# Optimization experiments

Hardware: AMD Instinct MI355X
Metric: run time of the kernel (lower is better)

Reference implementation:

```python
import jax, jax.numpy as jnp
import numpy as np

ODE_UNFOLDS = 6
EPS = 1e-8
MOTOR = 64  # wiring.output_dim


def setup_inputs() -> dict:
    key = jax.random.key(0)
    ks = jax.random.split(key, 16)
    B, S, U = 128, 128, 512  # batch, sensory_size, units
    d = {}
    d["inputs"] = jax.random.normal(ks[0], (B, S), jnp.float32)
    d["state"] = 0.1 * jax.random.normal(ks[1], (B, U), jnp.float32)
    # init ranges from LTCCell._init_ranges
    d["gleak"] = jax.random.uniform(ks[2], (U,), jnp.float32, 0.001, 1.0)
    d["vleak"] = jax.random.uniform(ks[3], (U,), jnp.float32, -0.2, 0.2)
    d["cm"] = jax.random.uniform(ks[4], (U,), jnp.float32, 0.4, 0.6)
    d["sigma"] = jax.random.uniform(ks[5], (U, U), jnp.float32, 3.0, 8.0)
    d["mu"] = jax.random.uniform(ks[6], (U, U), jnp.float32, 0.3, 0.8)
    d["w"] = jax.random.uniform(ks[7], (U, U), jnp.float32, 0.001, 1.0)
    d["erev"] = jnp.where(jax.random.uniform(ks[8], (U, U)) < 0.5, -1.0, 1.0).astype(jnp.float32)
    d["sensory_sigma"] = jax.random.uniform(ks[9], (S, U), jnp.float32, 3.0, 8.0)
    d["sensory_mu"] = jax.random.uniform(ks[10], (S, U), jnp.float32, 0.3, 0.8)
    d["sensory_w"] = jax.random.uniform(ks[11], (S, U), jnp.float32, 0.001, 1.0)
    d["sensory_erev"] = jnp.where(jax.random.uniform(ks[12], (S, U)) < 0.5, -1.0, 1.0).astype(jnp.float32)
    # affine input/output mapping params (initialized to identity as in build())
    d["input_w"] = jnp.ones((S,), jnp.float32)
    d["input_b"] = jnp.zeros((S,), jnp.float32)
    d["output_w"] = jnp.ones((MOTOR,), jnp.float32)
    d["output_b"] = jnp.zeros((MOTOR,), jnp.float32)
    d["sparsity_mask"] = (jax.random.uniform(ks[13], (U, U)) < 0.5).astype(jnp.float32)
    d["sensory_sparsity_mask"] = (jax.random.uniform(ks[14], (S, U)) < 0.5).astype(jnp.float32)
    return d


def reference(inputs, state, gleak, vleak, cm, sigma, mu, w, erev,
              sensory_sigma, sensory_mu, sensory_w, sensory_erev,
              input_w, input_b, output_w, output_b,
              sparsity_mask, sensory_sparsity_mask):
    # _map_inputs (affine)
    x = inputs * input_w + input_b  # [B, S]
    # sensory synapse activation (computed once, outside the unfold loop)
    # [B, S, U] = w * sigmoid((v_pre - mu) * sigma) * mask
    sens_act = sensory_w * jax.nn.sigmoid((x[:, :, None] - sensory_mu) * sensory_sigma) * sensory_sparsity_mask
    w_num_sensory = jnp.sum(sens_act * sensory_erev, axis=1)  # [B, U]
    w_den_sensory = jnp.sum(sens_act, axis=1)                 # [B, U]
    # cm_t = cm / (elapsed_time / ode_unfolds), elapsed_time = 1.0
    cm_t = cm * jnp.float32(ODE_UNFOLDS)

    def step(v_pre, _):
        # [B, U, U]
        act = w * jax.nn.sigmoid((v_pre[:, :, None] - mu) * sigma) * sparsity_mask
        w_num = jnp.sum(act * erev, axis=1) + w_num_sensory
        w_den = jnp.sum(act, axis=1) + w_den_sensory
        numerator = cm_t * v_pre + gleak * vleak + w_num
        denominator = cm_t + gleak + w_den
        return numerator / (denominator + EPS), None

    next_state, _ = jax.lax.scan(step, state, None, length=ODE_UNFOLDS)
    # _map_outputs: slice motor neurons, then affine
    outputs = next_state[:, :MOTOR] * output_w + output_b
    return outputs, next_state
```

## Files before the change

### kernel.cpp

```cpp
#include <hip/hip_runtime.h>

#define BATCH 128
#define SENS 128
#define UNITS 512
#define MOTOR 64
#define UNFOLDS 6
#define L2E 1.442695040888963f
#define EPS 1e-8f

#define BT 8
#define UT 8
#define STP 12

__global__ __launch_bounds__(256) void fold_kernel(
    const float* __restrict__ sigma, const float* __restrict__ mu,
    const float* __restrict__ w, const float* __restrict__ erev,
    const float* __restrict__ mask,
    const float* __restrict__ ssig, const float* __restrict__ smu,
    const float* __restrict__ sw, const float* __restrict__ serev,
    const float* __restrict__ smask,
    const float* __restrict__ inputs, const float* __restrict__ input_w,
    const float* __restrict__ input_b,
    float4* __restrict__ pw4, float4* __restrict__ ps4,
    float* __restrict__ x)
{
    int i = blockIdx.x * 256 + threadIdx.x;
    if (i < UNITS * UNITS) {
        float sg = sigma[i] * L2E;
        float wmv = w[i] * mask[i];
        float4 q;
        q.x = sg; q.y = mu[i] * sg; q.z = wmv; q.w = wmv * erev[i];
        pw4[i] = q;
    }
    if (i < SENS * UNITS) {
        float sg = ssig[i] * L2E;
        float wmv = sw[i] * smask[i];
        float4 q;
        q.x = sg; q.y = smu[i] * sg; q.z = wmv; q.w = wmv * serev[i];
        ps4[i] = q;
    }
    if (i < BATCH * SENS) {
        int s = i & (SENS - 1);
        x[i] = __builtin_fmaf(inputs[i], input_w[s], input_b[s]);
    }
}

__global__ __launch_bounds__(256, 4) void sensory_kernel(
    const float* __restrict__ x,
    const float4* __restrict__ ps4,
    float* __restrict__ wns, float* __restrict__ wds)
{
    __shared__ __align__(16) float xsT[SENS][STP];
    __shared__ float2 red[4][BT][UT];

    int phys = blockIdx.x;
    int logical = (phys & 7) * 128 + (phys >> 3);
    int ut = logical >> 4;
    int bt = logical & 15;
    int b0 = bt * BT;
    int u0 = ut * UT;

    {
        const float4* xv = (const float4*)(x + b0 * SENS);
        int bl = threadIdx.x & 7;
        int s4 = threadIdx.x >> 3;
        float4 t = xv[bl * (SENS / 4) + s4];
        xsT[s4 * 4 + 0][bl] = t.x;
        xsT[s4 * 4 + 1][bl] = t.y;
        xsT[s4 * 4 + 2][bl] = t.z;
        xsT[s4 * 4 + 3][bl] = t.w;
    }
    __syncthreads();

    int ul = threadIdx.x & 7;
    int ss = threadIdx.x >> 3;
    int u = u0 + ul;

    float num[BT], den[BT];
    #pragma unroll
    for (int b = 0; b < BT; ++b) { num[b] = 0.f; den[b] = 0.f; }

    const float4* pv = ps4 + (size_t)ss * UNITS + u;
    const float* srow = &xsT[ss][0];
    #pragma unroll
    for (int i = 0; i < SENS / 32; ++i) {
        float4 q = pv[0];
        pv += 32 * UNITS;
        const float4* sp = (const float4*)srow;
        float4 xa = sp[0];
        float4 xb = sp[1];
        srow += 32 * STP;
        float sarr[8] = {xa.x, xa.y, xa.z, xa.w, xb.x, xb.y, xb.z, xb.w};
        #pragma unroll
        for (int b = 0; b < BT; ++b) {
            float t = __builtin_fmaf(-sarr[b], q.x, q.y);
            float e = __builtin_amdgcn_exp2f(t);
            float sg = __builtin_amdgcn_rcpf(1.0f + e);
            num[b] = __builtin_fmaf(q.w, sg, num[b]);
            den[b] = __builtin_fmaf(q.z, sg, den[b]);
        }
    }

    #pragma unroll
    for (int b = 0; b < BT; ++b) {
        #pragma unroll
        for (int m = 8; m <= 32; m <<= 1) {
            num[b] += __shfl_xor(num[b], m, 64);
            den[b] += __shfl_xor(den[b], m, 64);
        }
    }
    int lane = threadIdx.x & 63;
    int wid = threadIdx.x >> 6;
    if (lane < 8) {
        #pragma unroll
        for (int b = 0; b < BT; ++b)
            red[wid][b][lane] = make_float2(num[b], den[b]);
    }
    __syncthreads();
    if (threadIdx.x < 64) {
        int uu = threadIdx.x & 7;
        int bb = threadIdx.x >> 3;
        float n = 0.f, d = 0.f;
        #pragma unroll
        for (int k = 0; k < 4; ++k) {
            float2 v = red[k][bb][uu];
            n += v.x; d += v.y;
        }
        int gidx = (b0 + bb) * UNITS + (u0 + uu);
        wns[gidx] = n;
        wds[gidx] = d;
    }
}

__global__ __launch_bounds__(256, 4) void unfold_kernel(
    const float* __restrict__ src,
    float* __restrict__ dst,
    const float4* __restrict__ pw4,
    const float* __restrict__ wns, const float* __restrict__ wds,
    const float* __restrict__ gleak, const float* __restrict__ vleak,
    const float* __restrict__ cm,
    const float* __restrict__ output_w, const float* __restrict__ output_b,
    float* __restrict__ out_motor,
    int last)
{
    __shared__ __align__(16) float stT[UNITS][STP];
    __shared__ float2 red[4][BT][UT];

    int phys = blockIdx.x;
    int logical = (phys & 7) * 128 + (phys >> 3);
    int ut = logical >> 4;
    int bt = logical & 15;
    int b0 = bt * BT;
    int u0 = ut * UT;

    {
        const float4* sv = (const float4*)(src + (size_t)b0 * UNITS);
        int bl = threadIdx.x & 7;
        int v4b = threadIdx.x >> 3;
        #pragma unroll
        for (int k = 0; k < 4; ++k) {
            int v4 = v4b + 32 * k;
            float4 t = sv[bl * (UNITS / 4) + v4];
            stT[v4 * 4 + 0][bl] = t.x;
            stT[v4 * 4 + 1][bl] = t.y;
            stT[v4 * 4 + 2][bl] = t.z;
            stT[v4 * 4 + 3][bl] = t.w;
        }
    }
    __syncthreads();

    int ul = threadIdx.x & 7;
    int vs = threadIdx.x >> 3;
    int u = u0 + ul;

    float num[BT], den[BT];
    #pragma unroll
    for (int b = 0; b < BT; ++b) { num[b] = 0.f; den[b] = 0.f; }

    const float4* pv = pw4 + (size_t)vs * UNITS + u;
    const float* srow = &stT[vs][0];
    #pragma unroll 4
    for (int i = 0; i < UNITS / 32; ++i) {
        float4 q = pv[0];
        pv += 32 * UNITS;
        const float4* sp = (const float4*)srow;
        float4 xa = sp[0];
        float4 xb = sp[1];
        srow += 32 * STP;
        float sarr[8] = {xa.x, xa.y, xa.z, xa.w, xb.x, xb.y, xb.z, xb.w};
        #pragma unroll
        for (int b = 0; b < BT; ++b) {
            float t = __builtin_fmaf(-sarr[b], q.x, q.y);
            float e = __builtin_amdgcn_exp2f(t);
            float sg = __builtin_amdgcn_rcpf(1.0f + e);
            num[b] = __builtin_fmaf(q.w, sg, num[b]);
            den[b] = __builtin_fmaf(q.z, sg, den[b]);
        }
    }

    #pragma unroll
    for (int b = 0; b < BT; ++b) {
        #pragma unroll
        for (int m = 8; m <= 32; m <<= 1) {
            num[b] += __shfl_xor(num[b], m, 64);
            den[b] += __shfl_xor(den[b], m, 64);
        }
    }
    int lane = threadIdx.x & 63;
    int wid = threadIdx.x >> 6;
    if (lane < 8) {
        #pragma unroll
        for (int b = 0; b < BT; ++b)
            red[wid][b][lane] = make_float2(num[b], den[b]);
    }
    __syncthreads();
    if (threadIdx.x < 64) {
        int uu = threadIdx.x & 7;
        int bb = threadIdx.x >> 3;
        float n = 0.f, d = 0.f;
        #pragma unroll
        for (int k = 0; k < 4; ++k) {
            float2 v = red[k][bb][uu];
            n += v.x; d += v.y;
        }
        int gu = u0 + uu;
        int gb = b0 + bb;
        float vpre = stT[gu][bb];
        float g = gleak[gu];
        float c = cm[gu] * (float)UNFOLDS;
        int gidx = gb * UNITS + gu;
        float numer = __builtin_fmaf(c, vpre,
                        __builtin_fmaf(g, vleak[gu], wns[gidx] + n));
        float denom = c + g + wds[gidx] + d + EPS;
        float res = numer * __builtin_amdgcn_rcpf(denom);
        dst[gidx] = res;
        if (last && gu < MOTOR) {
            out_motor[gb * MOTOR + gu] =
                __builtin_fmaf(res, output_w[gu], output_b[gu]);
        }
    }
}

extern "C" void kernel_launch(void* const* d_in, const int* in_sizes, int n_in,
                              void* d_out, int out_size, void* d_ws, size_t ws_size,
                              hipStream_t stream) {
    const float* inputs   = (const float*)d_in[0];
    const float* state    = (const float*)d_in[1];
    const float* gleak    = (const float*)d_in[2];
    const float* vleak    = (const float*)d_in[3];
    const float* cm       = (const float*)d_in[4];
    const float* sigma    = (const float*)d_in[5];
    const float* mu       = (const float*)d_in[6];
    const float* w        = (const float*)d_in[7];
    const float* erev     = (const float*)d_in[8];
    const float* ssig     = (const float*)d_in[9];
    const float* smu      = (const float*)d_in[10];
    const float* sw       = (const float*)d_in[11];
    const float* serev    = (const float*)d_in[12];
    const float* input_w  = (const float*)d_in[13];
    const float* input_b  = (const float*)d_in[14];
    const float* output_w = (const float*)d_in[15];
    const float* output_b = (const float*)d_in[16];
    const float* mask     = (const float*)d_in[17];
    const float* smask    = (const float*)d_in[18];

    float* out = (float*)d_out;
    float* ws  = (float*)d_ws;

    float4* pw4 = (float4*)ws;
    float4* ps4 = (float4*)(ws + 4 * UNITS * UNITS);
    float*  x   = ws + 4 * UNITS * UNITS + 4 * SENS * UNITS;
    float*  wns = x + BATCH * SENS;
    float*  wds = wns + BATCH * UNITS;
    float*  stA = wds + BATCH * UNITS;
    float*  stB = stA + BATCH * UNITS;

    fold_kernel<<<(UNITS * UNITS + 255) / 256, 256, 0, stream>>>(
        sigma, mu, w, erev, mask, ssig, smu, sw, serev, smask,
        inputs, input_w, input_b, pw4, ps4, x);

    sensory_kernel<<<1024, 256, 0, stream>>>(x, ps4, wns, wds);

    float* state_out = out + BATCH * MOTOR;
    float* dsts[UNFOLDS] = {stA, stB, stA, stB, stA, state_out};

    const float* src = state;
    for (int t = 0; t < UNFOLDS; ++t) {
        int last = (t == UNFOLDS - 1) ? 1 : 0;
        unfold_kernel<<<1024, 256, 0, stream>>>(
            src, dsts[t], pw4, wns, wds,
            gleak, vleak, cm, output_w, output_b, out, last);
        src = dsts[t];
    }
}
```

Baseline: 82.25 us.

## Compress recurrent synapses to per-unit sparse lists and fuse preprocessing kernels

A prep kernel now builds, for each postsynaptic unit, a compacted list of nonzero-mask synapses (folded sigma/mu/w/erev plus presynaptic index) using wave ballots. The unfold kernels iterate only over these entries, gathering presynaptic state rows from LDS, so roughly half of the exp/rcp work is skipped. The fold and sensory kernels are merged into that prep kernel, with the sensory parameters folded inline. The unfold reduction changes to a single-wave shuffle reduction, which removes the LDS reduction and the second barrier. Each list is capped at 352 entries, so a denser mask would silently drop synapses, and the indexed LDS gathers may cause bank conflicts.

```diff
diff --git a/kernel.cpp b/kernel.cpp
--- a/kernel.cpp
+++ b/kernel.cpp
@@ -11,96 +11,101 @@
 #define BT 8
 #define UT 8
 #define STP 12
-
-__global__ __launch_bounds__(256) void fold_kernel(
+#define MAXN 352
+
+__global__ __launch_bounds__(256, 4) void prep_kernel(
+    const float* __restrict__ inputs, const float* __restrict__ input_w,
+    const float* __restrict__ input_b,
+    const float* __restrict__ ssig, const float* __restrict__ smu,
+    const float* __restrict__ sw, const float* __restrict__ serev,
+    const float* __restrict__ smask,
     const float* __restrict__ sigma, const float* __restrict__ mu,
     const float* __restrict__ w, const float* __restrict__ erev,
     const float* __restrict__ mask,
-    const float* __restrict__ ssig, const float* __restrict__ smu,
-    const float* __restrict__ sw, const float* __restrict__ serev,
-    const float* __restrict__ smask,
-    const float* __restrict__ inputs, const float* __restrict__ input_w,
-    const float* __restrict__ input_b,
-    float4* __restrict__ pw4, float4* __restrict__ ps4,
-    float* __restrict__ x)
-{
-    int i = blockIdx.x * 256 + threadIdx.x;
-    if (i < UNITS * UNITS) {
-        float sg = sigma[i] * L2E;
-        float wmv = w[i] * mask[i];
-        float4 q;
-        q.x = sg; q.y = mu[i] * sg; q.z = wmv; q.w = wmv * erev[i];
-        pw4[i] = q;
-    }
-    if (i < SENS * UNITS) {
-        float sg = ssig[i] * L2E;
-        float wmv = sw[i] * smask[i];
-        float4 q;
-        q.x = sg; q.y = smu[i] * sg; q.z = wmv; q.w = wmv * serev[i];
-        ps4[i] = q;
-    }
-    if (i < BATCH * SENS) {
-        int s = i & (SENS - 1);
-        x[i] = __builtin_fmaf(inputs[i], input_w[s], input_b[s]);
-    }
-}
-
-__global__ __launch_bounds__(256, 4) void sensory_kernel(
-    const float* __restrict__ x,
-    const float4* __restrict__ ps4,
+    float4* __restrict__ qvA, int* __restrict__ idxA, int* __restrict__ cntA,
     float* __restrict__ wns, float* __restrict__ wds)
 {
     __shared__ __align__(16) float xsT[SENS][STP];
     __shared__ float2 red[4][BT][UT];
 
-    int phys = blockIdx.x;
-    int logical = (phys & 7) * 128 + (phys >> 3);
+    int tid = threadIdx.x;
+
+    if (blockIdx.x < 128) {
+        int wv = tid >> 6;
+        int lane = tid & 63;
+        int u = blockIdx.x * 4 + wv;
+        int slot = 0;
+        #pragma unroll
+        for (int vb = 0; vb < 8; ++vb) {
+            int v = vb * 64 + lane;
+            size_t k = (size_t)v * UNITS + u;
+            float mv = mask[k];
+            bool nz = (mv != 0.0f);
+            unsigned long long bal = __ballot(nz);
+            int pre = __popcll(bal & ((1ULL << lane) - 1ULL));
+            int s = slot + pre;
+            if (nz && s < MAXN) {
+                float sg = sigma[k] * L2E;
+                float wmv = w[k] * mv;
+                float4 q;
+                q.x = sg; q.y = mu[k] * sg; q.z = wmv; q.w = wmv * erev[k];
+                qvA[(size_t)u * MAXN + s] = q;
+                idxA[(size_t)u * MAXN + s] = v;
+            }
+            slot += __popcll(bal);
+        }
+        if (lane == 0) cntA[u] = (slot < MAXN) ? slot : MAXN;
+    }
+
+    int logical = (blockIdx.x & 7) * 128 + (blockIdx.x >> 3);
     int ut = logical >> 4;
     int bt = logical & 15;
     int b0 = bt * BT;
     int u0 = ut * UT;
 
     {
-        const float4* xv = (const float4*)(x + b0 * SENS);
-        int bl = threadIdx.x & 7;
-        int s4 = threadIdx.x >> 3;
-        float4 t = xv[bl * (SENS / 4) + s4];
-        xsT[s4 * 4 + 0][bl] = t.x;
-        xsT[s4 * 4 + 1][bl] = t.y;
-        xsT[s4 * 4 + 2][bl] = t.z;
-        xsT[s4 * 4 + 3][bl] = t.w;
+        int bl = tid & 7;
+        int s4 = tid >> 3;
+        const float4* xv = (const float4*)(inputs + (size_t)(b0 + bl) * SENS);
+        float4 t4 = xv[s4];
+        float4 iw = ((const float4*)input_w)[s4];
+        float4 ib = ((const float4*)input_b)[s4];
+        xsT[s4 * 4 + 0][bl] = __builtin_fmaf(t4.x, iw.x, ib.x);
+        xsT[s4 * 4 + 1][bl] = __builtin_fmaf(t4.y, iw.y, ib.y);
+        xsT[s4 * 4 + 2][bl] = __builtin_fmaf(t4.z, iw.z, ib.z);
+        xsT[s4 * 4 + 3][bl] = __builtin_fmaf(t4.w, iw.w, ib.w);
     }
     __syncthreads();
 
-    int ul = threadIdx.x & 7;
-    int ss = threadIdx.x >> 3;
+    int ul = tid & 7;
+    int grp = tid >> 3;
     int u = u0 + ul;
 
     float num[BT], den[BT];
     #pragma unroll
     for (int b = 0; b < BT; ++b) { num[b] = 0.f; den[b] = 0.f; }
 
-    const float4* pv = ps4 + (size_t)ss * UNITS + u;
-    const float* srow = &xsT[ss][0];
     #pragma unroll
     for (int i = 0; i < SENS / 32; ++i) {
-        float4 q = pv[0];
-        pv += 32 * UNITS;
-        const float4* sp = (const float4*)srow;
+        int s = grp + 32 * i;
+        size_t k = (size_t)s * UNITS + u;
+        float sgv = ssig[k] * L2E;
+        float mt  = smu[k] * sgv;
+        float wmv = sw[k] * smask[k];
+        float wev = wmv * serev[k];
+        const float4* sp = (const float4*)&xsT[s][0];
         float4 xa = sp[0];
         float4 xb = sp[1];
-        srow += 32 * STP;
         float sarr[8] = {xa.x, xa.y, xa.z, xa.w, xb.x, xb.y, xb.z, xb.w};
         #pragma unroll
         for (int b = 0; b < BT; ++b) {
-            float t = __builtin_fmaf(-sarr[b], q.x, q.y);
+            float t = __builtin_fmaf(-sarr[b], sgv, mt);
             float e = __builtin_amdgcn_exp2f(t);
             float sg = __builtin_amdgcn_rcpf(1.0f + e);
-            num[b] = __builtin_fmaf(q.w, sg, num[b]);
-            den[b] = __builtin_fmaf(q.z, sg, den[b]);
-        }
-    }
-
+            num[b] = __builtin_fmaf(wev, sg, num[b]);
+            den[b] = __builtin_fmaf(wmv, sg, den[b]);
+        }
+    }
     #pragma unroll
     for (int b = 0; b < BT; ++b) {
         #pragma unroll
@@ -109,17 +114,17 @@
             den[b] += __shfl_xor(den[b], m, 64);
         }
     }
-    int lane = threadIdx.x & 63;
-    int wid = threadIdx.x >> 6;
+    int lane = tid & 63;
+    int wid = tid >> 6;
     if (lane < 8) {
         #pragma unroll
         for (int b = 0; b < BT; ++b)
             red[wid][b][lane] = make_float2(num[b], den[b]);
     }
     __syncthreads();
-    if (threadIdx.x < 64) {
-        int uu = threadIdx.x & 7;
-        int bb = threadIdx.x >> 3;
+    if (tid < 64) {
+        int uu = tid & 7;
+        int bb = tid >> 3;
         float n = 0.f, d = 0.f;
         #pragma unroll
         for (int k = 0; k < 4; ++k) {
@@ -132,10 +137,11 @@
     }
 }
 
-__global__ __launch_bounds__(256, 4) void unfold_kernel(
+__global__ __launch_bounds__(256, 4) void unfold_sparse_kernel(
     const float* __restrict__ src,
     float* __restrict__ dst,
-    const float4* __restrict__ pw4,
+    const float4* __restrict__ qvA, const int* __restrict__ idxA,
+    const int* __restrict__ cntA,
     const float* __restrict__ wns, const float* __restrict__ wds,
     const float* __restrict__ gleak, const float* __restrict__ vleak,
     const float* __restrict__ cm,
@@ -144,55 +150,54 @@
     int last)
 {
     __shared__ __align__(16) float stT[UNITS][STP];
-    __shared__ float2 red[4][BT][UT];
-
-    int phys = blockIdx.x;
-    int logical = (phys & 7) * 128 + (phys >> 3);
+
+    int logical = (blockIdx.x & 7) * 128 + (blockIdx.x >> 3);
     int ut = logical >> 4;
     int bt = logical & 15;
     int b0 = bt * BT;
     int u0 = ut * UT;
+    int tid = threadIdx.x;
 
     {
         const float4* sv = (const float4*)(src + (size_t)b0 * UNITS);
-        int bl = threadIdx.x & 7;
-        int v4b = threadIdx.x >> 3;
+        int bl = tid & 7;
+        int v4b = tid >> 3;
         #pragma unroll
         for (int k = 0; k < 4; ++k) {
             int v4 = v4b + 32 * k;
-            float4 t = sv[bl * (UNITS / 4) + v4];
-            stT[v4 * 4 + 0][bl] = t.x;
-            stT[v4 * 4 + 1][bl] = t.y;
-            stT[v4 * 4 + 2][bl] = t.z;
-            stT[v4 * 4 + 3][bl] = t.w;
+            float4 t4 = sv[bl * (UNITS / 4) + v4];
+            stT[v4 * 4 + 0][bl] = t4.x;
+            stT[v4 * 4 + 1][bl] = t4.y;
+            stT[v4 * 4 + 2][bl] = t4.z;
+            stT[v4 * 4 + 3][bl] = t4.w;
         }
     }
     __syncthreads();
 
-    int ul = threadIdx.x & 7;
-    int vs = threadIdx.x >> 3;
+    int grp = tid & 31;
+    int ul  = tid >> 5;
     int u = u0 + ul;
+    int cnt_u = cntA[u];
+    const float4* qp = qvA + (size_t)u * MAXN;
+    const int*    ip = idxA + (size_t)u * MAXN;
 
     float num[BT], den[BT];
     #pragma unroll
     for (int b = 0; b < BT; ++b) { num[b] = 0.f; den[b] = 0.f; }
 
-    const float4* pv = pw4 + (size_t)vs * UNITS + u;
-    const float* srow = &stT[vs][0];
-    #pragma unroll 4
-    for (int i = 0; i < UNITS / 32; ++i) {
-        float4 q = pv[0];
-        pv += 32 * UNITS;
-        const float4* sp = (const float4*)srow;
-        float4 xa = sp[0];
-        float4 xb = sp[1];
-        srow += 32 * STP;
+    #pragma unroll 2
+    for (int e = grp; e < cnt_u; e += 32) {
+        float4 q = qp[e];
+        int vi = ip[e];
+        const float* srow = &stT[0][0] + vi * STP;
+        float4 xa = ((const float4*)srow)[0];
+        float4 xb = ((const float4*)srow)[1];
         float sarr[8] = {xa.x, xa.y, xa.z, xa.w, xb.x, xb.y, xb.z, xb.w};
         #pragma unroll
         for (int b = 0; b < BT; ++b) {
             float t = __builtin_fmaf(-sarr[b], q.x, q.y);
-            float e = __builtin_amdgcn_exp2f(t);
-            float sg = __builtin_amdgcn_rcpf(1.0f + e);
+            float e2 = __builtin_amdgcn_exp2f(t);
+            float sg = __builtin_amdgcn_rcpf(1.0f + e2);
             num[b] = __builtin_fmaf(q.w, sg, num[b]);
             den[b] = __builtin_fmaf(q.z, sg, den[b]);
         }
@@ -201,42 +206,31 @@
     #pragma unroll
     for (int b = 0; b < BT; ++b) {
         #pragma unroll
-        for (int m = 8; m <= 32; m <<= 1) {
+        for (int m = 1; m <= 16; m <<= 1) {
             num[b] += __shfl_xor(num[b], m, 64);
             den[b] += __shfl_xor(den[b], m, 64);
         }
     }
-    int lane = threadIdx.x & 63;
-    int wid = threadIdx.x >> 6;
-    if (lane < 8) {
-        #pragma unroll
-        for (int b = 0; b < BT; ++b)
-            red[wid][b][lane] = make_float2(num[b], den[b]);
-    }
-    __syncthreads();
-    if (threadIdx.x < 64) {
-        int uu = threadIdx.x & 7;
-        int bb = threadIdx.x >> 3;
-        float n = 0.f, d = 0.f;
-        #pragma unroll
-        for (int k = 0; k < 4; ++k) {
-            float2 v = red[k][bb][uu];
-            n += v.x; d += v.y;
-        }
-        int gu = u0 + uu;
-        int gb = b0 + bb;
-        float vpre = stT[gu][bb];
-        float g = gleak[gu];
-        float c = cm[gu] * (float)UNFOLDS;
-        int gidx = gb * UNITS + gu;
-        float numer = __builtin_fmaf(c, vpre,
-                        __builtin_fmaf(g, vleak[gu], wns[gidx] + n));
-        float denom = c + g + wds[gidx] + d + EPS;
-        float res = numer * __builtin_amdgcn_rcpf(denom);
-        dst[gidx] = res;
-        if (last && gu < MOTOR) {
-            out_motor[gb * MOTOR + gu] =
-                __builtin_fmaf(res, output_w[gu], output_b[gu]);
+
+    if (grp == 0) {
+        float g  = gleak[u];
+        float vl = vleak[u];
+        float c  = cm[u] * (float)UNFOLDS;
+        float ow = 0.f, ob = 0.f;
+        if (u < MOTOR) { ow = output_w[u]; ob = output_b[u]; }
+        #pragma unroll
+        for (int b = 0; b < BT; ++b) {
+            int gb = b0 + b;
+            int gidx = gb * UNITS + u;
+            float vpre = stT[u][b];
+            float numer = __builtin_fmaf(c, vpre,
+                            __builtin_fmaf(g, vl, wns[gidx] + num[b]));
+            float denom = c + g + wds[gidx] + den[b] + EPS;
+            float res = numer * __builtin_amdgcn_rcpf(denom);
+            dst[gidx] = res;
+            if (last && u < MOTOR) {
+                out_motor[gb * MOTOR + u] = __builtin_fmaf(res, ow, ob);
+            }
         }
     }
 }
@@ -267,19 +261,17 @@
     float* out = (float*)d_out;
     float* ws  = (float*)d_ws;
 
-    float4* pw4 = (float4*)ws;
-    float4* ps4 = (float4*)(ws + 4 * UNITS * UNITS);
-    float*  x   = ws + 4 * UNITS * UNITS + 4 * SENS * UNITS;
-    float*  wns = x + BATCH * SENS;
-    float*  wds = wns + BATCH * UNITS;
-    float*  stA = wds + BATCH * UNITS;
-    float*  stB = stA + BATCH * UNITS;
-
-    fold_kernel<<<(UNITS * UNITS + 255) / 256, 256, 0, stream>>>(
-        sigma, mu, w, erev, mask, ssig, smu, sw, serev, smask,
-        inputs, input_w, input_b, pw4, ps4, x);
-
-    sensory_kernel<<<1024, 256, 0, stream>>>(x, ps4, wns, wds);
+    float4* qvA  = (float4*)ws;
+    int*    idxA = (int*)(ws + 4 * UNITS * MAXN);
+    int*    cntA = (int*)(ws + 5 * UNITS * MAXN);
+    float*  wns  = ws + 5 * UNITS * MAXN + UNITS;
+    float*  wds  = wns + BATCH * UNITS;
+    float*  stA  = wds + BATCH * UNITS;
+    float*  stB  = stA + BATCH * UNITS;
+
+    prep_kernel<<<1024, 256, 0, stream>>>(
+        inputs, input_w, input_b, ssig, smu, sw, serev, smask,
+        sigma, mu, w, erev, mask, qvA, idxA, cntA, wns, wds);
 
     float* state_out = out + BATCH * MOTOR;
     float* dsts[UNFOLDS] = {stA, stB, stA, stB, stA, state_out};
@@ -287,8 +279,8 @@
     const float* src = state;
     for (int t = 0; t < UNFOLDS; ++t) {
         int last = (t == UNFOLDS - 1) ? 1 : 0;
-        unfold_kernel<<<1024, 256, 0, stream>>>(
-            src, dsts[t], pw4, wns, wds,
+        unfold_sparse_kernel<<<1024, 256, 0, stream>>>(
+            src, dsts[t], qvA, idxA, cntA, wns, wds,
             gleak, vleak, cm, output_w, output_b, out, last);
         src = dsts[t];
     }
```

After: 88.74 us. 1.08x slower.

## Fuse parameter folding, sensory reduction and first unfold step into one kernel

Applied to the files above, without the earlier changes.

Replaces the separate fold, sensory and first unfold kernels with a single kernel. It reads the raw sensory and recurrent parameters directly, computes the sensory sums, and performs the first ODE step. The packed recurrent parameter array is written as a side effect by only the bt==0 blocks, and the packed sensory array and the x buffer are dropped. This removes two launches and the round trip of the packed sensory data through memory. In exchange, each block redundantly reads five raw arrays instead of one packed float4 in the first step, and the remaining unfold launches depend on pw4 written within this kernel.

```diff
diff --git a/kernel.cpp b/kernel.cpp
--- a/kernel.cpp
+++ b/kernel.cpp
@@ -12,84 +12,132 @@
 #define UT 8
 #define STP 12
 
-__global__ __launch_bounds__(256) void fold_kernel(
+__global__ __launch_bounds__(256, 4) void unfold_first_kernel(
+    const float* __restrict__ inputs, const float* __restrict__ state,
     const float* __restrict__ sigma, const float* __restrict__ mu,
     const float* __restrict__ w, const float* __restrict__ erev,
     const float* __restrict__ mask,
     const float* __restrict__ ssig, const float* __restrict__ smu,
     const float* __restrict__ sw, const float* __restrict__ serev,
     const float* __restrict__ smask,
-    const float* __restrict__ inputs, const float* __restrict__ input_w,
-    const float* __restrict__ input_b,
-    float4* __restrict__ pw4, float4* __restrict__ ps4,
-    float* __restrict__ x)
+    const float* __restrict__ input_w, const float* __restrict__ input_b,
+    const float* __restrict__ gleak, const float* __restrict__ vleak,
+    const float* __restrict__ cm,
+    float4* __restrict__ pw4,
+    float* __restrict__ wns, float* __restrict__ wds,
+    float* __restrict__ dst)
 {
-    int i = blockIdx.x * 256 + threadIdx.x;
-    if (i < UNITS * UNITS) {
-        float sg = sigma[i] * L2E;
-        float wmv = w[i] * mask[i];
-        float4 q;
-        q.x = sg; q.y = mu[i] * sg; q.z = wmv; q.w = wmv * erev[i];
-        pw4[i] = q;
-    }
-    if (i < SENS * UNITS) {
-        float sg = ssig[i] * L2E;
-        float wmv = sw[i] * smask[i];
-        float4 q;
-        q.x = sg; q.y = smu[i] * sg; q.z = wmv; q.w = wmv * serev[i];
-        ps4[i] = q;
-    }
-    if (i < BATCH * SENS) {
-        int s = i & (SENS - 1);
-        x[i] = __builtin_fmaf(inputs[i], input_w[s], input_b[s]);
-    }
-}
-
-__global__ __launch_bounds__(256, 4) void sensory_kernel(
-    const float* __restrict__ x,
-    const float4* __restrict__ ps4,
-    float* __restrict__ wns, float* __restrict__ wds)
-{
+    __shared__ __align__(16) float stT[UNITS][STP];
     __shared__ __align__(16) float xsT[SENS][STP];
     __shared__ float2 red[4][BT][UT];
 
-    int phys = blockIdx.x;
-    int logical = (phys & 7) * 128 + (phys >> 3);
+    int tid = threadIdx.x;
+
+    int logical = (blockIdx.x & 7) * 128 + (blockIdx.x >> 3);
     int ut = logical >> 4;
     int bt = logical & 15;
     int b0 = bt * BT;
     int u0 = ut * UT;
 
+    int ul  = tid & 7;
+    int grp = tid >> 3;
+    int u = u0 + ul;
+    int lane = tid & 63;
+    int wid = tid >> 6;
+
     {
-        const float4* xv = (const float4*)(x + b0 * SENS);
-        int bl = threadIdx.x & 7;
-        int s4 = threadIdx.x >> 3;
-        float4 t = xv[bl * (SENS / 4) + s4];
-        xsT[s4 * 4 + 0][bl] = t.x;
-        xsT[s4 * 4 + 1][bl] = t.y;
-        xsT[s4 * 4 + 2][bl] = t.z;
-        xsT[s4 * 4 + 3][bl] = t.w;
-    }
-    __syncthreads();
-
-    int ul = threadIdx.x & 7;
-    int ss = threadIdx.x >> 3;
-    int u = u0 + ul;
+        int bl = tid & 7;
+        int v4b = tid >> 3;
+        const float4* sv = (const float4*)(state + (size_t)b0 * UNITS);
+        #pragma unroll
+        for (int k = 0; k < 4; ++k) {
+            int v4 = v4b + 32 * k;
+            float4 t4 = sv[bl * (UNITS / 4) + v4];
+            stT[v4 * 4 + 0][bl] = t4.x;
+            stT[v4 * 4 + 1][bl] = t4.y;
+            stT[v4 * 4 + 2][bl] = t4.z;
+            stT[v4 * 4 + 3][bl] = t4.w;
+        }
+        const float4* xv = (const float4*)(inputs + (size_t)(b0 + bl) * SENS);
+        float4 t4 = xv[v4b];
+        float4 iw = ((const float4*)input_w)[v4b];
+        float4 ib = ((const float4*)input_b)[v4b];
+        xsT[v4b * 4 + 0][bl] = __builtin_fmaf(t4.x, iw.x, ib.x);
+        xsT[v4b * 4 + 1][bl] = __builtin_fmaf(t4.y, iw.y, ib.y);
+        xsT[v4b * 4 + 2][bl] = __builtin_fmaf(t4.z, iw.z, ib.z);
+        xsT[v4b * 4 + 3][bl] = __builtin_fmaf(t4.w, iw.w, ib.w);
+    }
+    __syncthreads();
 
     float num[BT], den[BT];
     #pragma unroll
     for (int b = 0; b < BT; ++b) { num[b] = 0.f; den[b] = 0.f; }
 
-    const float4* pv = ps4 + (size_t)ss * UNITS + u;
-    const float* srow = &xsT[ss][0];
     #pragma unroll
     for (int i = 0; i < SENS / 32; ++i) {
-        float4 q = pv[0];
-        pv += 32 * UNITS;
-        const float4* sp = (const float4*)srow;
+        int s = grp + 32 * i;
+        size_t k = (size_t)s * UNITS + u;
+        float sgv = ssig[k] * L2E;
+        float mt  = smu[k] * sgv;
+        float wmv = sw[k] * smask[k];
+        float wev = wmv * serev[k];
+        const float4* sp = (const float4*)&xsT[s][0];
         float4 xa = sp[0];
         float4 xb = sp[1];
-        srow += 32 * STP;
+        float sarr[8] = {xa.x, xa.y, xa.z, xa.w, xb.x, xb.y, xb.z, xb.w};
+        #pragma unroll
+        for (int b = 0; b < BT; ++b) {
+            float t = __builtin_fmaf(-sarr[b], sgv, mt);
+            float e = __builtin_amdgcn_exp2f(t);
+            float sg = __builtin_amdgcn_rcpf(1.0f + e);
+            num[b] = __builtin_fmaf(wev, sg, num[b]);
+            den[b] = __builtin_fmaf(wmv, sg, den[b]);
+        }
+    }
+    #pragma unroll
+    for (int b = 0; b < BT; ++b) {
+        #pragma unroll
+        for (int m = 8; m <= 32; m <<= 1) {
+            num[b] += __shfl_xor(num[b], m, 64);
+            den[b] += __shfl_xor(den[b], m, 64);
+        }
+    }
+    if (lane < 8) {
+        #pragma unroll
+        for (int b = 0; b < BT; ++b)
+            red[wid][b][lane] = make_float2(num[b], den[b]);
+    }
+    __syncthreads();
+    float esn = 0.f, esd = 0.f;
+    if (tid < 64) {
+        int uu = tid & 7;
+        int bb = tid >> 3;
+        #pragma unroll
+        for (int k = 0; k < 4; ++k) {
+            float2 v = red[k][bb][uu];
+            esn += v.x; esd += v.y;
+        }
+        int gidx = (b0 + bb) * UNITS + (u0 + uu);
+        wns[gidx] = esn;
+        wds[gidx] = esd;
+    }
+    __syncthreads();
+
+    #pragma unroll
+    for (int b = 0; b < BT; ++b) { num[b] = 0.f; den[b] = 0.f; }
+
+    #pragma unroll 4
+    for (int i = 0; i < UNITS / 32; ++i) {
+        int v = grp + 32 * i;
+        size_t k = (size_t)v * UNITS + u;
+        float sgv = sigma[k] * L2E;
+        float wmv = w[k] * mask[k];
+        float4 q;
+        q.x = sgv; q.y = mu[k] * sgv; q.z = wmv; q.w = wmv * erev[k];
+        if (bt == 0) pw4[k] = q;
+        const float4* sp = (const float4*)&stT[v][0];
+        float4 xa = sp[0];
+        float4 xb = sp[1];
         float sarr[8] = {xa.x, xa.y, xa.z, xa.w, xb.x, xb.y, xb.z, xb.w};
         #pragma unroll
         for (int b = 0; b < BT; ++b) {
@@ -100,7 +148,6 @@
             den[b] = __builtin_fmaf(q.z, sg, den[b]);
         }
     }
-
     #pragma unroll
     for (int b = 0; b < BT; ++b) {
         #pragma unroll
@@ -109,26 +156,30 @@
             den[b] += __shfl_xor(den[b], m, 64);
         }
     }
-    int lane = threadIdx.x & 63;
-    int wid = threadIdx.x >> 6;
     if (lane < 8) {
         #pragma unroll
         for (int b = 0; b < BT; ++b)
             red[wid][b][lane] = make_float2(num[b], den[b]);
     }
     __syncthreads();
-    if (threadIdx.x < 64) {
-        int uu = threadIdx.x & 7;
-        int bb = threadIdx.x >> 3;
+    if (tid < 64) {
+        int uu = tid & 7;
+        int bb = tid >> 3;
         float n = 0.f, d = 0.f;
         #pragma unroll
         for (int k = 0; k < 4; ++k) {
             float2 v = red[k][bb][uu];
             n += v.x; d += v.y;
         }
-        int gidx = (b0 + bb) * UNITS + (u0 + uu);
-        wns[gidx] = n;
-        wds[gidx] = d;
+        int gu = u0 + uu;
+        int gb = b0 + bb;
+        float vpre = stT[gu][bb];
+        float g = gleak[gu];
+        float c = cm[gu] * (float)UNFOLDS;
+        float numer = __builtin_fmaf(c, vpre,
+                        __builtin_fmaf(g, vleak[gu], esn + n));
+        float denom = c + g + esd + d + EPS;
+        dst[gb * UNITS + gu] = numer * __builtin_amdgcn_rcpf(denom);
     }
 }
 
@@ -197,7 +248,6 @@
             den[b] = __builtin_fmaf(q.z, sg, den[b]);
         }
     }
-
     #pragma unroll
     for (int b = 0; b < BT; ++b) {
         #pragma unroll
@@ -268,25 +318,21 @@
     float* ws  = (float*)d_ws;
 
     float4* pw4 = (float4*)ws;
-    float4* ps4 = (float4*)(ws + 4 * UNITS * UNITS);
-    float*  x   = ws + 4 * UNITS * UNITS + 4 * SENS * UNITS;
-    float*  wns = x + BATCH * SENS;
+    float*  wns = ws + 4 * UNITS * UNITS;
     float*  wds = wns + BATCH * UNITS;
     float*  stA = wds + BATCH * UNITS;
     float*  stB = stA + BATCH * UNITS;
 
-    fold_kernel<<<(UNITS * UNITS + 255) / 256, 256, 0, stream>>>(
-        sigma, mu, w, erev, mask, ssig, smu, sw, serev, smask,
-        inputs, input_w, input_b, pw4, ps4, x);
-
-    sensory_kernel<<<1024, 256, 0, stream>>>(x, ps4, wns, wds);
+    unfold_first_kernel<<<1024, 256, 0, stream>>>(
+        inputs, state, sigma, mu, w, erev, mask,
+        ssig, smu, sw, serev, smask, input_w, input_b,
+        gleak, vleak, cm, pw4, wns, wds, stA);
 
     float* state_out = out + BATCH * MOTOR;
-    float* dsts[UNFOLDS] = {stA, stB, stA, stB, stA, state_out};
-
-    const float* src = state;
-    for (int t = 0; t < UNFOLDS; ++t) {
-        int last = (t == UNFOLDS - 1) ? 1 : 0;
+    float* dsts[5] = {stB, stA, stB, stA, state_out};
+    const float* src = stA;
+    for (int t = 0; t < 5; ++t) {
+        int last = (t == 4) ? 1 : 0;
         unfold_kernel<<<1024, 256, 0, stream>>>(
             src, dsts[t], pw4, wns, wds,
             gleak, vleak, cm, output_w, output_b, out, last);
```

After: 80.72 us. Within noise of the previous version (-1.9%).
